# Performance work log

Hardware: AMD Instinct MI355X
Metric: run time of the kernel (lower is better)

The kernel has to match this reference:

```python
import jax, jax.numpy as jnp
import numpy as np
from jax import lax

C, NH, HC, HID, P = 192, 8, 64, 512, 16
B, H, W = 2, 128, 128
EPS = 1e-5


def setup_inputs() -> dict:
    key = jax.random.key(0)
    ks = jax.random.split(key, 12)
    f = lambda i, shape: jax.random.normal(ks[i], shape, jnp.float32) * 0.05
    return dict(
        x=jax.random.normal(ks[0], (B, C, H, W), jnp.float32),
        ln1_g=jnp.ones((C,), jnp.float32), ln1_b=jnp.zeros((C,), jnp.float32),
        wq=f(1, (HID, C)), wk=f(2, (HID, C)), wv=f(3, (HID, C)),
        wo=f(4, (C, HID)), bo=jnp.zeros((C,), jnp.float32),
        dw_w=f(5, (C, 1, 3, 3)), dw_b=jnp.zeros((C,), jnp.float32),
        mlp_w=f(6, (C, 2 * C)), mlp_b=jnp.zeros((C,), jnp.float32),
        ln2_g=jnp.ones((C,), jnp.float32), ln2_b=jnp.zeros((C,), jnp.float32),
        c1_w=f(7, (C, C)), c1_b=jnp.zeros((C,), jnp.float32),
        res_w=f(8, (C, 1, 3, 3)), res_b=jnp.zeros((C,), jnp.float32),
        c2_w=f(9, (C, C)), c2_b=jnp.zeros((C,), jnp.float32),
    )


def ln_ch(x, g, b):
    # LayerNorm over the channel dim of an NCHW tensor (biased variance, like torch)
    m = x.mean(1, keepdims=True)
    v = ((x - m) ** 2).mean(1, keepdims=True)
    return (x - m) / jnp.sqrt(v + EPS) * g[None, :, None, None] + b[None, :, None, None]


def inorm(x):
    # InstanceNorm2d, affine=False
    m = x.mean((2, 3), keepdims=True)
    v = ((x - m) ** 2).mean((2, 3), keepdims=True)
    return (x - m) / jnp.sqrt(v + EPS)


def conv1x1(x, w, b=None):
    y = jnp.einsum('oc,bchw->bohw', w, x)
    return y if b is None else y + b[None, :, None, None]


def dwconv(x, w, b):
    y = lax.conv_general_dilated(x, w, (1, 1), 'SAME',
                                 feature_group_count=x.shape[1],
                                 dimension_numbers=('NCHW', 'OIHW', 'NCHW'))
    return y + b[None, :, None, None]


def res_block(x, w, b):
    return jax.nn.gelu(inorm(dwconv(x, w, b)), approximate=False) + x


def dpsa(x, ln_g, ln_b, wq, wk, wv, wo, bo):
    Bs, _, Hs, Ws = x.shape
    xn = ln_ch(x, ln_g, ln_b)

    def proj(w):  # -> (B*NH, H, W, HC)
        t = jnp.einsum('oc,bchw->bohw', w, xn)
        return t.reshape(Bs * NH, HC, Hs, Ws).transpose(0, 2, 3, 1)

    l2n = lambda t: t / jnp.maximum(jnp.linalg.norm(t, axis=-1, keepdims=True), 1e-12)
    q = l2n(proj(wq))
    k = l2n(proj(wk))
    v = proj(wv)

    qs = q.sum((1, 2))                                   # (BH, HC)
    h_scores = jnp.einsum('bc,bhc->bh', qs, k.sum(2))    # (BH, H)
    w_scores = jnp.einsum('bc,bwc->bw', qs, k.sum(1))    # (BH, W)
    _, h_idx = lax.top_k(h_scores, P)
    _, w_idx = lax.top_k(w_scores, P)

    k = jnp.take_along_axis(k, h_idx[:, :, None, None], axis=1)   # (BH, P, W, HC)
    v = jnp.take_along_axis(v, h_idx[:, :, None, None], axis=1)
    k = jnp.take_along_axis(k, w_idx[:, None, :, None], axis=2)   # (BH, P, P, HC)
    v = jnp.take_along_axis(v, w_idx[:, None, :, None], axis=2)

    qf = q.reshape(Bs * NH, Hs * Ws, HC)
    kf = k.reshape(Bs * NH, P * P, HC)
    vf = v.reshape(Bs * NH, P * P, HC)
    attn = jax.nn.softmax(jnp.einsum('bqc,bkc->bqk', qf, kf), axis=-1)
    out = jnp.einsum('bqk,bkc->bqc', attn, vf)
    out = out.reshape(Bs, NH, Hs, Ws, HC).transpose(0, 1, 4, 2, 3).reshape(Bs, NH * HC, Hs, Ws)
    return conv1x1(out, wo, bo)


def reference(x, ln1_g, ln1_b, wq, wk, wv, wo, bo, dw_w, dw_b, mlp_w, mlp_b,
              ln2_g, ln2_b, c1_w, c1_b, res_w, res_b, c2_w, c2_b):
    global_branch = dpsa(x, ln1_g, ln1_b, wq, wk, wv, wo, bo)
    local_branch = dwconv(x, dw_w, dw_b)
    f = jnp.concatenate((local_branch, global_branch), axis=1)
    f = conv1x1(f, mlp_w, mlp_b) + x
    y = ln_ch(f, ln2_g, ln2_b)
    y = jax.nn.gelu(inorm(conv1x1(y, c1_w, c1_b)), approximate=False)
    y = res_block(y, res_w, res_b)
    y = inorm(conv1x1(y, c2_w, c2_b))
    return y
```

## Files before the change

### kernel.cpp

```cpp
#include <hip/hip_runtime.h>
#include <math.h>

constexpr int kC   = 192;
constexpr int kNH  = 8;
constexpr int kHC  = 64;
constexpr int kHID = 512;
constexpr int kP   = 16;
constexpr int kB   = 2;
constexpr int kH   = 128;
constexpr int kW   = 128;
constexpr int kHW  = kH * kW;
constexpr int kN   = kB * kHW;
constexpr float kEPS = 1e-5f;

typedef __attribute__((ext_vector_type(8))) short bf16x8;
typedef __attribute__((ext_vector_type(4))) float f32x4;

__device__ inline unsigned short f2bf(float f) {
    unsigned int u = __builtin_bit_cast(unsigned int, f);
    unsigned int r = (u + 0x7FFFu + ((u >> 16) & 1u)) >> 16;
    return (unsigned short)r;
}
__device__ inline float bf2f(unsigned short u) {
    return __builtin_bit_cast(float, (unsigned int)u << 16);
}
__device__ inline unsigned int cvtpk(float lo, float hi) {
    unsigned int r;
    asm("v_cvt_pk_bf16_f32 %0, %1, %2" : "=v"(r) : "v"(lo), "v"(hi));
    return r;
}
__device__ inline unsigned long long pk4(float a, float b, float c, float d) {
    return (unsigned long long)cvtpk(a, b) | ((unsigned long long)cvtpk(c, d) << 32);
}
__device__ inline f32x4 ubf4(unsigned long long u) {
    f32x4 r;
    r[0] = bf2f((unsigned short)u);
    r[1] = bf2f((unsigned short)(u >> 16));
    r[2] = bf2f((unsigned short)(u >> 32));
    r[3] = bf2f((unsigned short)(u >> 48));
    return r;
}

__global__ void prep_kernel(float* __restrict__ acc,
                            const float* wq, const float* wk, const float* wm,
                            const float* c1, const float* c2,
                            unsigned short* wqb, unsigned short* wkb,
                            unsigned short* mlpb1, unsigned short* c1b, unsigned short* c2b)
{
    int i = blockIdx.x * 256 + threadIdx.x;
    if (i < 2304) { acc[i] = 0.f; return; }
    i -= 2304;
    if (i < 98304) { wqb[i] = f2bf(wq[i]); return; }
    i -= 98304;
    if (i < 98304) { wkb[i] = f2bf(wk[i]); return; }
    i -= 98304;
    if (i < 36864) { int o = i / 192, k = i - o * 192; mlpb1[i] = f2bf(wm[o * 384 + k]); return; }
    i -= 36864;
    if (i < 36864) { c1b[i] = f2bf(c1[i]); return; }
    i -= 36864;
    if (i < 36864) { c2b[i] = f2bf(c2[i]); return; }
}

__global__ void wfuse_kernel(const float* __restrict__ mlp_w, const float* __restrict__ wo,
                             const float* __restrict__ mlp_b, const float* __restrict__ bo,
                             unsigned short* __restrict__ w2pb, float* __restrict__ bp2)
{
    int i = blockIdx.x * 256 + threadIdx.x;
    int o = i >> 9, j = i & 511;
    const float* a = mlp_w + o * 384 + 192;
    float s = 0.f;
    for (int c = 0; c < 192; ++c) s += a[c] * wo[c * 512 + j];
    w2pb[o * 512 + j] = f2bf(s);
    if (j == 0) {
        float t = mlp_b[o];
        for (int c = 0; c < 192; ++c) t += a[c] * bo[c];
        bp2[o] = t;
    }
}

__global__ __launch_bounds__(256) void txln_kernel(const float* __restrict__ x,
                                                   float* __restrict__ xp,
                                                   unsigned short* __restrict__ xnb,
                                                   const float* __restrict__ g,
                                                   const float* __restrict__ bb)
{
    __shared__ float tile[192][65];
    __shared__ float red[2][4][64];
    __shared__ float pms[64], prs[64];
    int hw0 = blockIdx.x * 64;
    int b   = blockIdx.y;
    int tid = threadIdx.x;
    for (int i = tid; i < 192 * 64; i += 256) {
        int c = i >> 6, p = i & 63;
        tile[c][p] = x[(size_t)(b * kC + c) * kHW + hw0 + p];
    }
    __syncthreads();
    {
        int p = tid & 63, qt = tid >> 6;
        float s = 0.f, ss = 0.f;
        for (int c = qt * 48; c < qt * 48 + 48; ++c) {
            float v = tile[c][p]; s += v; ss += v * v;
        }
        red[0][qt][p] = s; red[1][qt][p] = ss;
    }
    __syncthreads();
    if (tid < 64) {
        float s  = red[0][0][tid] + red[0][1][tid] + red[0][2][tid] + red[0][3][tid];
        float ss = red[1][0][tid] + red[1][1][tid] + red[1][2][tid] + red[1][3][tid];
        float m = s * (1.0f / kC);
        float var = ss * (1.0f / kC) - m * m;
        pms[tid] = m;
        prs[tid] = rsqrtf(var + kEPS);
    }
    __syncthreads();
    for (int i = tid; i < 64 * 192; i += 256) {
        int p = i / 192, c = i - p * 192;
        float raw = tile[c][p];
        size_t oi = (size_t)(b * kHW + hw0 + p) * kC + c;
        xp[oi] = raw;
        xnb[oi] = f2bf((raw - pms[p]) * prs[p] * g[c] + bb[c]);
    }
}

__global__ void ln_pm_bf16_kernel(const unsigned short* __restrict__ in,
                                  unsigned short* __restrict__ out,
                                  const float* __restrict__ g, const float* __restrict__ bb)
{
    int n = blockIdx.x * 256 + threadIdx.x;
    if (n >= kN) return;
    const unsigned long long* ip = (const unsigned long long*)(in + (size_t)n * kC);
    float s = 0.f, ss = 0.f;
    f32x4 vals[48];
#pragma unroll
    for (int r = 0; r < 48; ++r) {
        f32x4 v = ubf4(ip[r]);
        vals[r] = v;
        s  += (v[0] + v[1]) + (v[2] + v[3]);
        ss += (v[0]*v[0] + v[1]*v[1]) + (v[2]*v[2] + v[3]*v[3]);
    }
    float m  = s * (1.0f / kC);
    float var = ss * (1.0f / kC) - m * m;
    float rs = rsqrtf(var + kEPS);
    unsigned long long* op = (unsigned long long*)(out + (size_t)n * kC);
#pragma unroll
    for (int r = 0; r < 48; ++r) {
        f32x4 v = vals[r];
        f32x4 gg = *(const f32x4*)(g + r * 4);
        f32x4 bv = *(const f32x4*)(bb + r * 4);
        op[r] = pk4((v[0]-m)*rs*gg[0] + bv[0], (v[1]-m)*rs*gg[1] + bv[1],
                    (v[2]-m)*rs*gg[2] + bv[2], (v[3]-m)*rs*gg[3] + bv[3]);
    }
}

#define MGEMM_CORE(KVAL, APTR, BPTR)                                              \
    {                                                                             \
        const unsigned short* Ap = APTR;                                          \
        const unsigned short* Bp = BPTR;                                          \
        _Pragma("unroll 2")                                                       \
        for (int k = 0; k < KVAL; k += 32) {                                      \
            bf16x8 a0 = *(const bf16x8*)(Ap + k);                                 \
            bf16x8 a1 = *(const bf16x8*)(Ap + (size_t)16 * KVAL + k);             \
            bf16x8 b0 = *(const bf16x8*)(Bp + k);                                 \
            bf16x8 b1 = *(const bf16x8*)(Bp + (size_t)16 * KVAL + k);             \
            bf16x8 b2 = *(const bf16x8*)(Bp + (size_t)32 * KVAL + k);             \
            bf16x8 b3 = *(const bf16x8*)(Bp + (size_t)48 * KVAL + k);             \
            acc[0][0] = __builtin_amdgcn_mfma_f32_16x16x32_bf16(a0, b0, acc[0][0], 0, 0, 0); \
            acc[0][1] = __builtin_amdgcn_mfma_f32_16x16x32_bf16(a0, b1, acc[0][1], 0, 0, 0); \
            acc[0][2] = __builtin_amdgcn_mfma_f32_16x16x32_bf16(a0, b2, acc[0][2], 0, 0, 0); \
            acc[0][3] = __builtin_amdgcn_mfma_f32_16x16x32_bf16(a0, b3, acc[0][3], 0, 0, 0); \
            acc[1][0] = __builtin_amdgcn_mfma_f32_16x16x32_bf16(a1, b0, acc[1][0], 0, 0, 0); \
            acc[1][1] = __builtin_amdgcn_mfma_f32_16x16x32_bf16(a1, b1, acc[1][1], 0, 0, 0); \
            acc[1][2] = __builtin_amdgcn_mfma_f32_16x16x32_bf16(a1, b2, acc[1][2], 0, 0, 0); \
            acc[1][3] = __builtin_amdgcn_mfma_f32_16x16x32_bf16(a1, b3, acc[1][3], 0, 0, 0); \
        }                                                                         \
    }

__global__ __launch_bounds__(256) void mgemm_is_kernel(
    const unsigned short* __restrict__ A, const unsigned short* __restrict__ B,
    unsigned short* __restrict__ out, const float* __restrict__ bias,
    float* __restrict__ accp)
{
    __shared__ float sa[2][64], qa[2][64];
    int nB = blockIdx.x * 128, oB = blockIdx.y * 64;
    int w = threadIdx.x >> 6, lane = threadIdx.x & 63;
    int l15 = lane & 15, g = lane >> 4;
    int wm = w & 1, wn = w >> 1;

    f32x4 acc[2][4];
#pragma unroll
    for (int mt = 0; mt < 2; ++mt)
#pragma unroll
        for (int nt = 0; nt < 4; ++nt) acc[mt][nt] = (f32x4){0.f,0.f,0.f,0.f};

    MGEMM_CORE(192, A + (size_t)(oB + wm * 32 + l15) * 192 + 8 * g,
                    B + (size_t)(nB + wn * 64 + l15) * 192 + 8 * g);

    f32x4 vv[2][4];
#pragma unroll
    for (int mt = 0; mt < 2; ++mt)
#pragma unroll
        for (int nt = 0; nt < 4; ++nt) {
            int o = oB + wm * 32 + mt * 16 + 4 * g;
            int n = nB + wn * 64 + nt * 16 + l15;
            f32x4 v = acc[mt][nt] + *(const f32x4*)(bias + o);
            vv[mt][nt] = v;
            *(unsigned long long*)(out + (size_t)n * kC + o) = pk4(v[0], v[1], v[2], v[3]);
        }
    float s2[2][4] = {}, q2[2][4] = {};
#pragma unroll
    for (int mt = 0; mt < 2; ++mt)
#pragma unroll
        for (int nt = 0; nt < 4; ++nt)
#pragma unroll
            for (int r = 0; r < 4; ++r) {
                float v = vv[mt][nt][r];
                s2[mt][r] += v; q2[mt][r] += v * v;
            }
#pragma unroll
    for (int off = 1; off < 16; off <<= 1)
#pragma unroll
        for (int mt = 0; mt < 2; ++mt)
#pragma unroll
            for (int r = 0; r < 4; ++r) {
                s2[mt][r] += __shfl_xor(s2[mt][r], off);
                q2[mt][r] += __shfl_xor(q2[mt][r], off);
            }
    if (l15 == 0)
#pragma unroll
        for (int mt = 0; mt < 2; ++mt)
#pragma unroll
            for (int r = 0; r < 4; ++r) {
                int ol = wm * 32 + mt * 16 + 4 * g + r;
                sa[wn][ol] = s2[mt][r];
                qa[wn][ol] = q2[mt][r];
            }
    __syncthreads();
    if (threadIdx.x < 128) {
        int ol = threadIdx.x & 63, st = threadIdx.x >> 6;
        float v = st ? (qa[0][ol] + qa[1][ol]) : (sa[0][ol] + sa[1][ol]);
        int b = nB >> 14;
        atomicAdd(&accp[(size_t)(b * kC + oB + ol) * 2 + st], v);
    }
}

__global__ __launch_bounds__(256) void mgemm_mlp_kernel(
    const unsigned short* __restrict__ A1, const unsigned short* __restrict__ B1,
    const unsigned short* __restrict__ A2, const unsigned short* __restrict__ B2,
    unsigned short* __restrict__ out, const float* __restrict__ bp2,
    const float* __restrict__ res)
{
    int nB = blockIdx.x * 128, oB = blockIdx.y * 64;
    int w = threadIdx.x >> 6, lane = threadIdx.x & 63;
    int l15 = lane & 15, g = lane >> 4;
    int wm = w & 1, wn = w >> 1;

    f32x4 acc[2][4];
#pragma unroll
    for (int mt = 0; mt < 2; ++mt)
#pragma unroll
        for (int nt = 0; nt < 4; ++nt) acc[mt][nt] = (f32x4){0.f,0.f,0.f,0.f};

    MGEMM_CORE(192, A1 + (size_t)(oB + wm * 32 + l15) * 192 + 8 * g,
                    B1 + (size_t)(nB + wn * 64 + l15) * 192 + 8 * g);
    MGEMM_CORE(512, A2 + (size_t)(oB + wm * 32 + l15) * 512 + 8 * g,
                    B2 + (size_t)(nB + wn * 64 + l15) * 512 + 8 * g);

#pragma unroll
    for (int mt = 0; mt < 2; ++mt)
#pragma unroll
        for (int nt = 0; nt < 4; ++nt) {
            int o = oB + wm * 32 + mt * 16 + 4 * g;
            int n = nB + wn * 64 + nt * 16 + l15;
            f32x4 v = acc[mt][nt];
            v[0] += bp2[o]; v[1] += bp2[o+1]; v[2] += bp2[o+2]; v[3] += bp2[o+3];
            v += *(const f32x4*)(res + (size_t)n * kC + o);
            *(unsigned long long*)(out + (size_t)n * kC + o) = pk4(v[0], v[1], v[2], v[3]);
        }
}

__global__ __launch_bounds__(256) void mgemm_l2_kernel(
    const unsigned short* __restrict__ A, const unsigned short* __restrict__ B,
    unsigned short* __restrict__ out, float* __restrict__ red_out)
{
    __shared__ float ssq[2][2][4][16];
    __shared__ float rbuf[2][2][4][2][4];
    int nB = blockIdx.x * 128, oB = blockIdx.y * 64;
    int w = threadIdx.x >> 6, lane = threadIdx.x & 63;
    int l15 = lane & 15, g = lane >> 4;
    int wm = w & 1, wn = w >> 1;

    f32x4 acc[2][4];
#pragma unroll
    for (int mt = 0; mt < 2; ++mt)
#pragma unroll
        for (int nt = 0; nt < 4; ++nt) acc[mt][nt] = (f32x4){0.f,0.f,0.f,0.f};

    MGEMM_CORE(192, A + (size_t)(oB + wm * 32 + l15) * 192 + 8 * g,
                    B + (size_t)(nB + wn * 64 + l15) * 192 + 8 * g);

#pragma unroll
    for (int nt = 0; nt < 4; ++nt) {
        float s = 0.f;
#pragma unroll
        for (int mt = 0; mt < 2; ++mt) {
            f32x4 a = acc[mt][nt];
            s += (a[0]*a[0] + a[1]*a[1]) + (a[2]*a[2] + a[3]*a[3]);
        }
        s += __shfl_xor(s, 16);
        s += __shfl_xor(s, 32);
        if (g == 0) ssq[wm][wn][nt][l15] = s;
    }
    __syncthreads();

    float sc[4];
#pragma unroll
    for (int nt = 0; nt < 4; ++nt) {
        float ss2 = ssq[0][wn][nt][l15] + ssq[1][wn][nt][l15];
        sc[nt] = 1.0f / fmaxf(sqrtf(ss2), 1e-12f);
    }

#pragma unroll
    for (int nt = 0; nt < 4; ++nt) {
        int n = nB + wn * 64 + nt * 16 + l15;
#pragma unroll
        for (int mt = 0; mt < 2; ++mt) {
            int o = oB + wm * 32 + mt * 16 + 4 * g;
            f32x4 v = acc[mt][nt];
            *(unsigned long long*)(out + (size_t)n * kHID + o) =
                pk4(v[0]*sc[nt], v[1]*sc[nt], v[2]*sc[nt], v[3]*sc[nt]);
        }
    }

    float sred[2][4] = {};
#pragma unroll
    for (int nt = 0; nt < 4; ++nt)
#pragma unroll
        for (int mt = 0; mt < 2; ++mt) {
            f32x4 a = acc[mt][nt];
            sred[mt][0] += a[0] * sc[nt];
            sred[mt][1] += a[1] * sc[nt];
            sred[mt][2] += a[2] * sc[nt];
            sred[mt][3] += a[3] * sc[nt];
        }
#pragma unroll
    for (int off = 1; off < 16; off <<= 1)
#pragma unroll
        for (int mt = 0; mt < 2; ++mt)
#pragma unroll
            for (int r = 0; r < 4; ++r)
                sred[mt][r] += __shfl_xor(sred[mt][r], off);
    if (l15 == 0)
#pragma unroll
        for (int mt = 0; mt < 2; ++mt)
#pragma unroll
            for (int r = 0; r < 4; ++r)
                rbuf[wm][wn][g][mt][r] = sred[mt][r];
    __syncthreads();
    if (threadIdx.x < 64) {
        int o = threadIdx.x;
        int wm2 = o >> 5, mt2 = (o >> 4) & 1, g2 = (o >> 2) & 3, r2 = o & 3;
        float v = rbuf[wm2][0][g2][mt2][r2] + rbuf[wm2][1][g2][mt2][r2];
        int row = (nB & (kHW - 1)) >> 7;
        int b = nB >> 14;
        int bh = b * 8 + blockIdx.y;
        red_out[((size_t)(bh * 128 + row)) * 64 + o] = v;
    }
}

__global__ void sum_h_kernel(const unsigned short* __restrict__ buf, float* __restrict__ out)
{
    int w = blockIdx.x, bh = blockIdx.y, hc = threadIdx.x;
    int b = bh >> 3, nh = bh & 7;
    const unsigned short* p = buf + (size_t)(b * kHW + w) * kHID + nh * kHC + hc;
    float s = 0.f;
    for (int h = 0; h < kH; ++h) s += bf2f(p[(size_t)h * kW * kHID]);
    out[((size_t)bh * kW + w) * kHC + hc] = s;
}

__global__ void score_topk_kernel(const float* __restrict__ qpart,
                                  const float* __restrict__ ksum_h,
                                  const float* __restrict__ ksum_w,
                                  int* __restrict__ hidx, int* __restrict__ widx)
{
    __shared__ float qsl[2][64];
    __shared__ float hs[128], ws[128];
    int bh = blockIdx.x;
    int tid = threadIdx.x;
    int hc = tid & 63, grp = tid >> 6;
    {
        const float* qp = qpart + ((size_t)bh * 128 + grp * 64) * 64 + hc;
        float s = 0.f;
        for (int i = 0; i < 64; ++i) s += qp[(size_t)i * 64];
        qsl[grp][hc] = s;
    }
    __syncthreads();
    if (tid < 64) qsl[0][tid] += qsl[1][tid];
    __syncthreads();
    {
        const float* kh = ksum_h + ((size_t)bh * 128 + tid) * 64;
        const float* kw = ksum_w + ((size_t)bh * 128 + tid) * 64;
        float sh = 0.f, sw = 0.f;
        for (int c = 0; c < 64; ++c) {
            float q = qsl[0][c];
            sh += q * kh[c];
            sw += q * kw[c];
        }
        hs[tid] = sh; ws[tid] = sw;
    }
    __syncthreads();
    int sel = tid >> 6;
    const float* sc = sel ? ws : hs;
    int* out = (sel ? widx : hidx) + bh * kP;
    int lane = tid & 63;
    float v0 = sc[lane], v1 = sc[lane + 64];
    int i0 = lane, i1 = lane + 64;
    for (int p = 0; p < kP; ++p) {
        float bv; int bi;
        if (v1 > v0) { bv = v1; bi = i1; } else { bv = v0; bi = i0; }
#pragma unroll
        for (int off = 1; off < 64; off <<= 1) {
            float ov = __shfl_xor(bv, off);
            int   oi = __shfl_xor(bi, off);
            if (ov > bv || (ov == bv && oi < bi)) { bv = ov; bi = oi; }
        }
        if (lane == 0) out[p] = bi;
        if (i0 == bi) v0 = -INFINITY;
        if (i1 == bi) v1 = -INFINITY;
    }
}

__global__ void gather_kv_kernel(const unsigned short* __restrict__ kpb,
                                 const unsigned short* __restrict__ xnb,
                                 const float* __restrict__ wv,
                                 const int* __restrict__ hidx, const int* __restrict__ widx,
                                 unsigned short* __restrict__ kf, unsigned short* __restrict__ vfT)
{
    int bh = blockIdx.y, p1 = blockIdx.x;
    int b = bh >> 3, nh = bh & 7;
    int hc = threadIdx.x & 63, pg = threadIdx.x >> 6;
    int hrow = hidx[bh * kP + p1];
    int o = nh * kHC + hc;
    const float* wvp = wv + (size_t)o * kC;
    for (int p2 = pg; p2 < kP; p2 += 4) {
        int wcol = widx[bh * kP + p2];
        int n = b * kHW + hrow * kW + wcol;
        int kidx = p1 * kP + p2;
        kf[((size_t)bh * 256 + kidx) * 64 + hc] = kpb[(size_t)n * kHID + nh * kHC + hc];
        const unsigned int* xr = (const unsigned int*)(xnb + (size_t)n * kC);
        float s = 0.f;
        for (int c2 = 0; c2 < kC / 2; ++c2) {
            unsigned int u = xr[c2];
            s += wvp[c2 * 2]     * bf2f((unsigned short)(u & 0xffff));
            s += wvp[c2 * 2 + 1] * bf2f((unsigned short)(u >> 16));
        }
        vfT[((size_t)bh * 64 + hc) * 256 + kidx] = f2bf(s);
    }
}

__global__ __launch_bounds__(256) void attn_kernel(
    const unsigned short* __restrict__ qpb, unsigned short* __restrict__ ob,
    const unsigned short* __restrict__ kf, const unsigned short* __restrict__ vfT)
{
    __shared__ unsigned short pls[64 * 136];
    __shared__ float lred[4][4][16];

    int bh = blockIdx.y; int b = bh >> 3, nh = bh & 7;
    int n0 = b * kHW + blockIdx.x * 64;
    int tid = threadIdx.x;
    int w = tid >> 6, lane = tid & 63, l15 = lane & 15, g = lane >> 4;

    bf16x8 bq[4][2];
#pragma unroll
    for (int nt = 0; nt < 4; ++nt)
#pragma unroll
        for (int kt = 0; kt < 2; ++kt)
            bq[nt][kt] = *(const bf16x8*)(qpb + (size_t)(n0 + nt * 16 + l15) * kHID
                                          + nh * kHC + kt * 32 + 8 * g);

    const unsigned short* kfb = kf + (size_t)bh * 256 * 64;
    bf16x8 ak[4][2];
#pragma unroll
    for (int mt = 0; mt < 4; ++mt)
#pragma unroll
        for (int kt = 0; kt < 2; ++kt)
            ak[mt][kt] = *(const bf16x8*)&kfb[(size_t)(w * 64 + mt * 16 + l15) * 64 + kt * 32 + 8 * g];

    f32x4 acc[4][4];
#pragma unroll
    for (int mt = 0; mt < 4; ++mt)
#pragma unroll
        for (int nt = 0; nt < 4; ++nt) acc[mt][nt] = (f32x4){0.f,0.f,0.f,0.f};

#pragma unroll
    for (int kt = 0; kt < 2; ++kt)
#pragma unroll
        for (int mt = 0; mt < 4; ++mt)
#pragma unroll
            for (int nt = 0; nt < 4; ++nt)
                acc[mt][nt] = __builtin_amdgcn_mfma_f32_16x16x32_bf16(
                    ak[mt][kt], bq[nt][kt], acc[mt][nt], 0, 0, 0);

    float lpart[4] = {0.f, 0.f, 0.f, 0.f};
#pragma unroll
    for (int mt = 0; mt < 4; ++mt)
#pragma unroll
        for (int nt = 0; nt < 4; ++nt) {
            float e0 = __expf(acc[mt][nt][0]);
            float e1 = __expf(acc[mt][nt][1]);
            float e2 = __expf(acc[mt][nt][2]);
            float e3 = __expf(acc[mt][nt][3]);
            lpart[nt] += (e0 + e1) + (e2 + e3);
            if (w < 2) {
                int qq = nt * 16 + l15;
                int k0 = (w & 1) * 64 + mt * 16 + 4 * g;
                *(unsigned long long*)&pls[qq * 136 + k0] = pk4(e0, e1, e2, e3);
            }
        }
#pragma unroll
    for (int nt = 0; nt < 4; ++nt) {
        lpart[nt] += __shfl_xor(lpart[nt], 16);
        lpart[nt] += __shfl_xor(lpart[nt], 32);
    }
    if (g == 0)
#pragma unroll
        for (int nt = 0; nt < 4; ++nt) lred[w][nt][l15] = lpart[nt];
    __syncthreads();

    const unsigned short* vfb = vfT + (size_t)bh * 64 * 256;
    f32x4 oacc[4];
#pragma unroll
    for (int nt = 0; nt < 4; ++nt) oacc[nt] = (f32x4){0.f,0.f,0.f,0.f};

#pragma unroll
    for (int ks = 0; ks < 4; ++ks) {
        bf16x8 av = *(const bf16x8*)&vfb[(size_t)(w * 16 + l15) * 256 + ks * 32 + 8 * g];
#pragma unroll
        for (int nt = 0; nt < 4; ++nt) {
            bf16x8 bp = *(const bf16x8*)&pls[(nt * 16 + l15) * 136 + ks * 32 + 8 * g];
            oacc[nt] = __builtin_amdgcn_mfma_f32_16x16x32_bf16(av, bp, oacc[nt], 0, 0, 0);
        }
    }
    __syncthreads();
    if (w >= 2) {
#pragma unroll
        for (int mt = 0; mt < 4; ++mt)
#pragma unroll
            for (int nt = 0; nt < 4; ++nt) {
                float e0 = __expf(acc[mt][nt][0]);
                float e1 = __expf(acc[mt][nt][1]);
                float e2 = __expf(acc[mt][nt][2]);
                float e3 = __expf(acc[mt][nt][3]);
                int qq = nt * 16 + l15;
                int k0 = (w & 1) * 64 + mt * 16 + 4 * g;
                *(unsigned long long*)&pls[qq * 136 + k0] = pk4(e0, e1, e2, e3);
            }
    }
    __syncthreads();
#pragma unroll
    for (int ks = 0; ks < 4; ++ks) {
        bf16x8 av = *(const bf16x8*)&vfb[(size_t)(w * 16 + l15) * 256 + 128 + ks * 32 + 8 * g];
#pragma unroll
        for (int nt = 0; nt < 4; ++nt) {
            bf16x8 bp = *(const bf16x8*)&pls[(nt * 16 + l15) * 136 + ks * 32 + 8 * g];
            oacc[nt] = __builtin_amdgcn_mfma_f32_16x16x32_bf16(av, bp, oacc[nt], 0, 0, 0);
        }
    }

#pragma unroll
    for (int nt = 0; nt < 4; ++nt) {
        float l = lred[0][nt][l15] + lred[1][nt][l15] + lred[2][nt][l15] + lred[3][nt][l15];
        float inv = 1.0f / l;
        int qq = nt * 16 + l15;
        int hc0 = w * 16 + 4 * g;
        *(unsigned long long*)(ob + (size_t)(n0 + qq) * kHID + nh * kHC + hc0) =
            pk4(oacc[nt][0] * inv, oacc[nt][1] * inv, oacc[nt][2] * inv, oacc[nt][3] * inv);
    }
}

template<int INBF16>
__global__ void dwconv_pm_kernel(const void* __restrict__ in, unsigned short* __restrict__ out,
                                 const float* __restrict__ wt, const float* __restrict__ bias)
{
    int idx = blockIdx.x * 256 + threadIdx.x;
    int n = idx / 48;
    int c0 = (idx - n * 48) * 4;
    int hw = n & (kHW - 1);
    int h = hw >> 7, ww = hw & 127;
    f32x4 s = *(const f32x4*)(bias + c0);
#pragma unroll
    for (int dy = -1; dy <= 1; ++dy) {
        int hh = h + dy;
        if (hh < 0 || hh >= kH) continue;
#pragma unroll
        for (int dx = -1; dx <= 1; ++dx) {
            int wx = ww + dx;
            if (wx < 0 || wx >= kW) continue;
            f32x4 v;
            if (INBF16)
                v = ubf4(*(const unsigned long long*)((const unsigned short*)in
                          + (size_t)(n + dy * kW + dx) * kC + c0));
            else
                v = *(const f32x4*)((const float*)in + (size_t)(n + dy * kW + dx) * kC + c0);
            int t = (dy + 1) * 3 + (dx + 1);
            s[0] += v[0] * wt[(c0 + 0) * 9 + t];
            s[1] += v[1] * wt[(c0 + 1) * 9 + t];
            s[2] += v[2] * wt[(c0 + 2) * 9 + t];
            s[3] += v[3] * wt[(c0 + 3) * 9 + t];
        }
    }
    *(unsigned long long*)(out + (size_t)n * kC + c0) = pk4(s[0], s[1], s[2], s[3]);
}

__global__ void istats_bf16_kernel(const unsigned short* __restrict__ in, float* __restrict__ acc)
{
    int n0 = blockIdx.x * 64;
    int b = n0 >> 14;
    int c = threadIdx.x;
    float s = 0.f, ss = 0.f;
    for (int p = 0; p < 64; ++p) {
        float v = bf2f(in[(size_t)(n0 + p) * kC + c]);
        s += v; ss += v * v;
    }
    atomicAdd(&acc[(size_t)(b * kC + c) * 2],     s);
    atomicAdd(&acc[(size_t)(b * kC + c) * 2 + 1], ss);
}

__device__ inline void inorm_ms(const float* acc, int b, int c, float& m, float& rs)
{
    float s  = acc[(size_t)(b * kC + c) * 2];
    float ss = acc[(size_t)(b * kC + c) * 2 + 1];
    m = s * (1.0f / kHW);
    float var = ss * (1.0f / kHW) - m * m;
    rs = rsqrtf(var + kEPS);
}

template<int MODE>
__global__ void apply_pm_kernel(const unsigned short* __restrict__ in, const float* __restrict__ acc,
                                unsigned short* __restrict__ out, const unsigned short* __restrict__ addsrc)
{
    int idx = blockIdx.x * 256 + threadIdx.x;
    int n = idx / 48;
    int c0 = (idx - n * 48) * 4;
    int b = n >> 14;
    f32x4 v = ubf4(*(const unsigned long long*)(in + (size_t)n * kC + c0));
    f32x4 r;
#pragma unroll
    for (int j = 0; j < 4; ++j) {
        float m, rs;
        inorm_ms(acc, b, c0 + j, m, rs);
        float x = (v[j] - m) * rs;
        r[j] = 0.5f * x * (1.0f + erff(x * 0.70710678118654752f));
    }
    if (MODE == 1)
        r += ubf4(*(const unsigned long long*)(addsrc + (size_t)n * kC + c0));
    *(unsigned long long*)(out + (size_t)n * kC + c0) = pk4(r[0], r[1], r[2], r[3]);
}

__global__ void final_kernel(const unsigned short* __restrict__ in, const float* __restrict__ acc,
                             float* __restrict__ out)
{
    int id = blockIdx.x * 256 + threadIdx.x;
    int oid = id * 4;
    int q = oid >> 14;
    int hw = oid & (kHW - 1);
    int b = (q >= kC) ? 1 : 0;
    int c = q - b * kC;
    float m, rs;
    inorm_ms(acc, b, c, m, rs);
    int n = b * kHW + hw;
    f32x4 o;
#pragma unroll
    for (int j = 0; j < 4; ++j)
        o[j] = (bf2f(in[(size_t)(n + j) * kC + c]) - m) * rs;
    *(f32x4*)(out + (size_t)oid) = o;
}

extern "C" void kernel_launch(void* const* d_in, const int* in_sizes, int n_in,
                              void* d_out, int out_size, void* d_ws, size_t ws_size,
                              hipStream_t stream)
{
    const float* x     = (const float*)d_in[0];
    const float* ln1_g = (const float*)d_in[1];
    const float* ln1_b = (const float*)d_in[2];
    const float* wq    = (const float*)d_in[3];
    const float* wk    = (const float*)d_in[4];
    const float* wv    = (const float*)d_in[5];
    const float* wo    = (const float*)d_in[6];
    const float* bo    = (const float*)d_in[7];
    const float* dw_w  = (const float*)d_in[8];
    const float* dw_b  = (const float*)d_in[9];
    const float* mlp_w = (const float*)d_in[10];
    const float* mlp_b = (const float*)d_in[11];
    const float* ln2_g = (const float*)d_in[12];
    const float* ln2_b = (const float*)d_in[13];
    const float* c1_w  = (const float*)d_in[14];
    const float* c1_b  = (const float*)d_in[15];
    const float* res_w = (const float*)d_in[16];
    const float* res_b = (const float*)d_in[17];
    const float* c2_w  = (const float*)d_in[18];
    const float* c2_b  = (const float*)d_in[19];

    char* base = (char*)d_ws;
    float* XP = (float*)(base);
    unsigned short* XNb = (unsigned short*)(base + 25165824);
    unsigned short* QPb = (unsigned short*)(base + 37748736);
    unsigned short* F   = QPb;
    unsigned short* T2  = QPb;
    unsigned short* KPb = (unsigned short*)(base + 71303168);
    unsigned short* OB  = KPb;
    unsigned short* Y2  = KPb;
    unsigned short* LB  = (unsigned short*)(base + 104857600);
    unsigned short* Y3  = LB;
    unsigned short* T1  = (unsigned short*)(base + 117440512);
    unsigned short* R   = T1;
    char* sm = base + 130023424;
    float* qpart  = (float*)(sm);                 sm += 524288;
    float* ksum_h = (float*)(sm);                 sm += 524288;
    float* ksum_w = (float*)(sm);                 sm += 524288;
    float* acc0   = (float*)(sm);                 sm += 3072;
    float* acc1   = (float*)(sm);                 sm += 3072;
    float* acc2   = (float*)(sm);                 sm += 3072;
    unsigned short* kf   = (unsigned short*)(sm); sm += 524288;
    unsigned short* vfT  = (unsigned short*)(sm); sm += 524288;
    unsigned short* wqb  = (unsigned short*)(sm); sm += 196608;
    unsigned short* wkb  = (unsigned short*)(sm); sm += 196608;
    unsigned short* mlpb1= (unsigned short*)(sm); sm += 73728;
    unsigned short* c1b  = (unsigned short*)(sm); sm += 73728;
    unsigned short* c2b  = (unsigned short*)(sm); sm += 73728;
    unsigned short* w2pb = (unsigned short*)(sm); sm += 196608;
    float* bp2 = (float*)(sm);                    sm += 1024;
    int* hidx = (int*)(sm);                       sm += 1024;
    int* widx = (int*)(sm);

    prep_kernel<<<1209, 256, 0, stream>>>(acc0, wq, wk, mlp_w, c1_w, c2_w,
                                          wqb, wkb, mlpb1, c1b, c2b);
    wfuse_kernel<<<384, 256, 0, stream>>>(mlp_w, wo, mlp_b, bo, w2pb, bp2);
    txln_kernel<<<dim3(kHW / 64, kB), 256, 0, stream>>>(x, XP, XNb, ln1_g, ln1_b);

    mgemm_l2_kernel<<<dim3(kN / 128, kNH), 256, 0, stream>>>(wqb, XNb, QPb, qpart);
    mgemm_l2_kernel<<<dim3(kN / 128, kNH), 256, 0, stream>>>(wkb, XNb, KPb, ksum_h);
    sum_h_kernel<<<dim3(kW, 16), 64, 0, stream>>>(KPb, ksum_w);
    score_topk_kernel<<<16, 128, 0, stream>>>(qpart, ksum_h, ksum_w, hidx, widx);
    gather_kv_kernel<<<dim3(kP, 16), 256, 0, stream>>>(KPb, XNb, wv, hidx, widx, kf, vfT);
    attn_kernel<<<dim3(kHW / 64, 16), 256, 0, stream>>>(QPb, OB, kf, vfT);

    dwconv_pm_kernel<0><<<(kN * 48) / 256, 256, 0, stream>>>(XP, LB, dw_w, dw_b);
    mgemm_mlp_kernel<<<dim3(kN / 128, kC / 64), 256, 0, stream>>>(mlpb1, LB, w2pb, OB, F, bp2, XP);

    ln_pm_bf16_kernel<<<kN / 256, 256, 0, stream>>>(F, XNb, ln2_g, ln2_b);
    mgemm_is_kernel<<<dim3(kN / 128, kC / 64), 256, 0, stream>>>(c1b, XNb, T1, c1_b, acc0);
    apply_pm_kernel<0><<<(kN * 48) / 256, 256, 0, stream>>>(T1, acc0, Y2, nullptr);
    dwconv_pm_kernel<1><<<(kN * 48) / 256, 256, 0, stream>>>(Y2, R, res_w, res_b);
    istats_bf16_kernel<<<kN / 64, 192, 0, stream>>>(R, acc1);
    apply_pm_kernel<1><<<(kN * 48) / 256, 256, 0, stream>>>(R, acc1, Y3, Y2);
    mgemm_is_kernel<<<dim3(kN / 128, kC / 64), 256, 0, stream>>>(c2b, Y3, T2, c2_b, acc2);
    final_kernel<<<(kC * kN / 4) / 256, 256, 0, stream>>>(T2, acc2, (float*)d_out);
}
```

Before: 546.0 us.

## Transpose final output via LDS tile, single-pass attention P buffer, reload LN inputs

The final kernel now stages a 64-pixel by 192-channel bf16 tile in shared memory, so the global reads from pixel-major storage are coalesced before the channel-major fp32 output is written. Before, each thread read single strided bf16 values. The attention kernel doubles its shared P buffer so all four waves write their exponentials at once. This removes the two-phase PV product and its extra barriers and recomputed exps, at the cost of more LDS per block and possibly lower occupancy. The LN kernel no longer keeps 48 vectors in registers and rereads the input instead, trading register pressure for a second (likely cached) read.

```diff
diff --git a/kernel.cpp b/kernel.cpp
--- a/kernel.cpp
+++ b/kernel.cpp
@@ -130,11 +130,9 @@
     if (n >= kN) return;
     const unsigned long long* ip = (const unsigned long long*)(in + (size_t)n * kC);
     float s = 0.f, ss = 0.f;
-    f32x4 vals[48];
 #pragma unroll
     for (int r = 0; r < 48; ++r) {
         f32x4 v = ubf4(ip[r]);
-        vals[r] = v;
         s  += (v[0] + v[1]) + (v[2] + v[3]);
         ss += (v[0]*v[0] + v[1]*v[1]) + (v[2]*v[2] + v[3]*v[3]);
     }
@@ -144,7 +142,7 @@
     unsigned long long* op = (unsigned long long*)(out + (size_t)n * kC);
 #pragma unroll
     for (int r = 0; r < 48; ++r) {
-        f32x4 v = vals[r];
+        f32x4 v = ubf4(ip[r]);
         f32x4 gg = *(const f32x4*)(g + r * 4);
         f32x4 bv = *(const f32x4*)(bb + r * 4);
         op[r] = pk4((v[0]-m)*rs*gg[0] + bv[0], (v[1]-m)*rs*gg[1] + bv[1],
@@ -461,7 +459,7 @@
     const unsigned short* __restrict__ qpb, unsigned short* __restrict__ ob,
     const unsigned short* __restrict__ kf, const unsigned short* __restrict__ vfT)
 {
-    __shared__ unsigned short pls[64 * 136];
+    __shared__ unsigned short pls[64 * 272];
     __shared__ float lred[4][4][16];
 
     int bh = blockIdx.y; int b = bh >> 3, nh = bh & 7;
@@ -510,11 +508,9 @@
             float e2 = __expf(acc[mt][nt][2]);
             float e3 = __expf(acc[mt][nt][3]);
             lpart[nt] += (e0 + e1) + (e2 + e3);
-            if (w < 2) {
-                int qq = nt * 16 + l15;
-                int k0 = (w & 1) * 64 + mt * 16 + 4 * g;
-                *(unsigned long long*)&pls[qq * 136 + k0] = pk4(e0, e1, e2, e3);
-            }
+            int qq = nt * 16 + l15;
+            int k0 = w * 64 + mt * 16 + 4 * g;
+            *(unsigned long long*)&pls[qq * 272 + k0] = pk4(e0, e1, e2, e3);
         }
 #pragma unroll
     for (int nt = 0; nt < 4; ++nt) {
@@ -532,36 +528,11 @@
     for (int nt = 0; nt < 4; ++nt) oacc[nt] = (f32x4){0.f,0.f,0.f,0.f};
 
 #pragma unroll
-    for (int ks = 0; ks < 4; ++ks) {
+    for (int ks = 0; ks < 8; ++ks) {
         bf16x8 av = *(const bf16x8*)&vfb[(size_t)(w * 16 + l15) * 256 + ks * 32 + 8 * g];
 #pragma unroll
         for (int nt = 0; nt < 4; ++nt) {
-            bf16x8 bp = *(const bf16x8*)&pls[(nt * 16 + l15) * 136 + ks * 32 + 8 * g];
-            oacc[nt] = __builtin_amdgcn_mfma_f32_16x16x32_bf16(av, bp, oacc[nt], 0, 0, 0);
-        }
-    }
-    __syncthreads();
-    if (w >= 2) {
-#pragma unroll
-        for (int mt = 0; mt < 4; ++mt)
-#pragma unroll
-            for (int nt = 0; nt < 4; ++nt) {
-                float e0 = __expf(acc[mt][nt][0]);
-                float e1 = __expf(acc[mt][nt][1]);
-                float e2 = __expf(acc[mt][nt][2]);
-                float e3 = __expf(acc[mt][nt][3]);
-                int qq = nt * 16 + l15;
-                int k0 = (w & 1) * 64 + mt * 16 + 4 * g;
-                *(unsigned long long*)&pls[qq * 136 + k0] = pk4(e0, e1, e2, e3);
-            }
-    }
-    __syncthreads();
-#pragma unroll
-    for (int ks = 0; ks < 4; ++ks) {
-        bf16x8 av = *(const bf16x8*)&vfb[(size_t)(w * 16 + l15) * 256 + 128 + ks * 32 + 8 * g];
-#pragma unroll
-        for (int nt = 0; nt < 4; ++nt) {
-            bf16x8 bp = *(const bf16x8*)&pls[(nt * 16 + l15) * 136 + ks * 32 + 8 * g];
+            bf16x8 bp = *(const bf16x8*)&pls[(nt * 16 + l15) * 272 + ks * 32 + 8 * g];
             oacc[nt] = __builtin_amdgcn_mfma_f32_16x16x32_bf16(av, bp, oacc[nt], 0, 0, 0);
         }
     }
@@ -656,23 +627,34 @@
     *(unsigned long long*)(out + (size_t)n * kC + c0) = pk4(r[0], r[1], r[2], r[3]);
 }
 
-__global__ void final_kernel(const unsigned short* __restrict__ in, const float* __restrict__ acc,
-                             float* __restrict__ out)
-{
-    int id = blockIdx.x * 256 + threadIdx.x;
-    int oid = id * 4;
-    int q = oid >> 14;
-    int hw = oid & (kHW - 1);
-    int b = (q >= kC) ? 1 : 0;
-    int c = q - b * kC;
-    float m, rs;
-    inorm_ms(acc, b, c, m, rs);
-    int n = b * kHW + hw;
-    f32x4 o;
-#pragma unroll
-    for (int j = 0; j < 4; ++j)
-        o[j] = (bf2f(in[(size_t)(n + j) * kC + c]) - m) * rs;
-    *(f32x4*)(out + (size_t)oid) = o;
+__global__ __launch_bounds__(256) void final_kernel(const unsigned short* __restrict__ in,
+                                                    const float* __restrict__ acc,
+                                                    float* __restrict__ out)
+{
+    __shared__ unsigned short tile[192][68];
+    int n0 = blockIdx.x * 64;
+    int b = n0 >> 14;
+    int hw0 = n0 & (kHW - 1);
+    int tid = threadIdx.x;
+    for (int i = tid; i < 64 * 48; i += 256) {
+        int p = i / 48, cq = i - p * 48;
+        unsigned long long u = *(const unsigned long long*)(in + (size_t)(n0 + p) * kC + cq * 4);
+        tile[cq * 4 + 0][p] = (unsigned short)u;
+        tile[cq * 4 + 1][p] = (unsigned short)(u >> 16);
+        tile[cq * 4 + 2][p] = (unsigned short)(u >> 32);
+        tile[cq * 4 + 3][p] = (unsigned short)(u >> 48);
+    }
+    __syncthreads();
+    for (int i = tid; i < 192 * 16; i += 256) {
+        int c = i >> 4, grp = i & 15;
+        float m, rs;
+        inorm_ms(acc, b, c, m, rs);
+        f32x4 o;
+#pragma unroll
+        for (int j = 0; j < 4; ++j)
+            o[j] = (bf2f(tile[c][grp * 4 + j]) - m) * rs;
+        *(f32x4*)(out + (size_t)(b * kC + c) * kHW + hw0 + grp * 4) = o;
+    }
 }
 
 extern "C" void kernel_launch(void* const* d_in, const int* in_sizes, int n_in,
@@ -754,5 +736,5 @@
     istats_bf16_kernel<<<kN / 64, 192, 0, stream>>>(R, acc1);
     apply_pm_kernel<1><<<(kN * 48) / 256, 256, 0, stream>>>(R, acc1, Y3, Y2);
     mgemm_is_kernel<<<dim3(kN / 128, kC / 64), 256, 0, stream>>>(c2b, Y3, T2, c2_b, acc2);
-    final_kernel<<<(kC * kN / 4) / 256, 256, 0, stream>>>(T2, acc2, (float*)d_out);
-}
+    final_kernel<<<kN / 64, 256, 0, stream>>>(T2, acc2, (float*)d_out);
+}
```

Result: faster. 497.2 us (-8.9%).
